# Kernel optimization log

Measured on AMD Instinct MI355X. Metric: run time of the kernel, lower is better.

Reference implementation:

```python
import jax, jax.numpy as jnp
import numpy as np

LAMBDA_LAME = 1.0
MU_LAME = 0.5
JACOBIAN_WEIGHT = 0.1
ERROR_BOUND = 0.01


def setup_inputs() -> dict:
    key = jax.random.key(0)
    df = jax.random.normal(key, (2, 3, 192, 192, 192), dtype=jnp.float32)
    return {"deformation_field": df}


def _grad(x, axis):
    # matches torch.gradient / np.gradient (edge_order=1): central diff in the
    # interior, one-sided first-order at the boundaries, unit spacing.
    return jnp.gradient(x, axis=axis)


def _robust(x, delta):
    abs_x = jnp.abs(x)
    return jnp.where(abs_x <= delta, 0.5 * x * x, delta * (abs_x - 0.5 * delta))


def reference(deformation_field):
    u = deformation_field[:, 0]  # [B, D, H, W]
    v = deformation_field[:, 1]
    w = deformation_field[:, 2]

    du_dx, du_dy, du_dz = _grad(u, 1), _grad(u, 2), _grad(u, 3)
    dv_dx, dv_dy, dv_dz = _grad(v, 1), _grad(v, 2), _grad(v, 3)
    dw_dx, dw_dy, dw_dz = _grad(w, 1), _grad(w, 2), _grad(w, 3)

    E_xx, E_yy, E_zz = du_dx, dv_dy, dw_dz
    E_xy = 0.5 * (du_dy + dv_dx)
    E_xz = 0.5 * (du_dz + dw_dx)
    E_yz = 0.5 * (dv_dz + dw_dy)
    trace_E = E_xx + E_yy + E_zz

    d = ERROR_BOUND
    tr_l = _robust(trace_E, d)
    energy = (0.5 * LAMBDA_LAME * tr_l ** 2
              + MU_LAME * (_robust(E_xx, d) ** 2 + _robust(E_yy, d) ** 2
                           + _robust(E_zz, d) ** 2
                           + 2.0 * (_robust(E_xy, d) ** 2
                                    + _robust(E_xz, d) ** 2
                                    + _robust(E_yz, d) ** 2)))

    jac = ((1 + du_dx) * ((1 + dv_dy) * (1 + dw_dz) - dv_dz * dw_dy)
           - du_dy * (dv_dx * (1 + dw_dz) - dv_dz * (1 + dw_dx))
           + du_dz * (dv_dx * dw_dy - (1 + dv_dy) * (1 + dw_dx)))
    jac_penalty = jax.nn.relu(-jac)

    total = jnp.mean(energy) + JACOBIAN_WEIGHT * jnp.mean(jac_penalty)
    return total
```

## Files before the change

kernel.cpp:

```cpp
#include <hip/hip_runtime.h>

#define DIM 192
#define PLANE (DIM * DIM)
#define VOL ((size_t)PLANE * DIM)

__device__ __forceinline__ float robustf(float x) {
    float ax = fabsf(x);
    return (ax <= 0.01f) ? (0.5f * x * x) : (0.01f * (ax - 0.005f));
}

__device__ __forceinline__ float4 ldg4(const float* __restrict__ p) {
    return *(const float4*)p;
}

__device__ __forceinline__ float4 sub_scale(float4 a, float4 b, float s) {
    return make_float4((a.x - b.x) * s, (a.y - b.y) * s,
                       (a.z - b.z) * s, (a.w - b.w) * s);
}

__device__ __forceinline__ float voxel_loss(
    float du_dx, float du_dy, float du_dz,
    float dv_dx, float dv_dy, float dv_dz,
    float dw_dx, float dw_dy, float dw_dz) {
    const float E_xy = 0.5f * (du_dy + dv_dx);
    const float E_xz = 0.5f * (du_dz + dw_dx);
    const float E_yz = 0.5f * (dv_dz + dw_dy);
    const float tr   = du_dx + dv_dy + dw_dz;

    const float rtr = robustf(tr);
    const float rxx = robustf(du_dx), ryy = robustf(dv_dy), rzz = robustf(dw_dz);
    const float rxy = robustf(E_xy),  rxz = robustf(E_xz),  ryz = robustf(E_yz);

    const float energy = 0.5f * rtr * rtr
                       + 0.5f * (rxx * rxx + ryy * ryy + rzz * rzz
                                 + 2.0f * (rxy * rxy + rxz * rxz + ryz * ryz));

    const float jac =
          (1.0f + du_dx) * ((1.0f + dv_dy) * (1.0f + dw_dz) - dv_dz * dw_dy)
        - du_dy * (dv_dx * (1.0f + dw_dz) - dv_dz * (1.0f + dw_dx))
        + du_dz * (dv_dx * dw_dy - (1.0f + dv_dy) * (1.0f + dw_dx));

    return energy + 0.1f * fmaxf(-jac, 0.0f);
}

__device__ __forceinline__ float4 zgrad(float4 c, float lf, float rt,
                                        bool leftEdge, bool rightEdge) {
    float4 g;
    g.x = leftEdge  ? (c.y - c.x) : 0.5f * (c.y - lf);
    g.y = 0.5f * (c.z - c.x);
    g.z = 0.5f * (c.w - c.y);
    g.w = rightEdge ? (c.w - c.z) : 0.5f * (rt - c.z);
    return g;
}

__global__ __launch_bounds__(256, 4)
void elastic_main(const float* __restrict__ df, double* __restrict__ acc) {
    const int tx = threadIdx.x;
    const int ty = threadIdx.y;
    const int k4 = tx * 4;
    const int j  = blockIdx.x * 4 + ty;
    const int i0 = blockIdx.y * 24;
    const int b  = blockIdx.z;

    const float* __restrict__ u = df + (size_t)(b * 3 + 0) * VOL;
    const float* __restrict__ v = df + (size_t)(b * 3 + 1) * VOL;
    const float* __restrict__ w = df + (size_t)(b * 3 + 2) * VOL;

    const int jp = (j < DIM - 1) ? j + 1 : j;
    const int jm = (j > 0) ? j - 1 : j;
    const float sy = ((jp - jm) == 2) ? 0.5f : 1.0f;

    const bool act = (tx < 48);
    const bool leftEdge  = (tx == 0);
    const bool rightEdge = (tx == 47);

    float4 um, vm, wm, uc, vc, wc;
    um = vm = wm = uc = vc = wc = make_float4(0.f, 0.f, 0.f, 0.f);

    {
        const int im1 = (i0 > 0) ? i0 - 1 : 0;
        const size_t oM = (size_t)im1 * PLANE + (size_t)j * DIM + k4;
        const size_t oC = (size_t)i0  * PLANE + (size_t)j * DIM + k4;
        if (act) {
            um = ldg4(u + oM); vm = ldg4(v + oM); wm = ldg4(w + oM);
            uc = ldg4(u + oC); vc = ldg4(v + oC); wc = ldg4(w + oC);
        }
    }

    float vsum = 0.0f;

    for (int ii = 0; ii < 24; ++ii) {
        const int i   = i0 + ii;
        const int ip1 = (i < DIM - 1) ? i + 1 : i;
        const int im1 = (i > 0) ? i - 1 : i;
        const float sx = ((ip1 - im1) == 2) ? 0.5f : 1.0f;

        const size_t oP  = (size_t)ip1 * PLANE + (size_t)j  * DIM + k4;
        const size_t oYp = (size_t)i   * PLANE + (size_t)jp * DIM + k4;
        const size_t oYm = (size_t)i   * PLANE + (size_t)jm * DIM + k4;

        float4 up, vp, wp, uyp, uym, vyp, vym, wyp, wym;
        up = vp = wp = make_float4(0.f, 0.f, 0.f, 0.f);
        if (act) {
            up  = ldg4(u + oP);  vp  = ldg4(v + oP);  wp  = ldg4(w + oP);
            uyp = ldg4(u + oYp); uym = ldg4(u + oYm);
            vyp = ldg4(v + oYp); vym = ldg4(v + oYm);
            wyp = ldg4(w + oYp); wym = ldg4(w + oYm);
        }

        const float ulf = __shfl_up(uc.w, 1);
        const float vlf = __shfl_up(vc.w, 1);
        const float wlf = __shfl_up(wc.w, 1);
        const float urt = __shfl_down(uc.x, 1);
        const float vrt = __shfl_down(vc.x, 1);
        const float wrt = __shfl_down(wc.x, 1);

        if (act) {
            const float4 du_dz = zgrad(uc, ulf, urt, leftEdge, rightEdge);
            const float4 dv_dz = zgrad(vc, vlf, vrt, leftEdge, rightEdge);
            const float4 dw_dz = zgrad(wc, wlf, wrt, leftEdge, rightEdge);

            const float4 du_dx = sub_scale(up, um, sx);
            const float4 dv_dx = sub_scale(vp, vm, sx);
            const float4 dw_dx = sub_scale(wp, wm, sx);
            const float4 du_dy = sub_scale(uyp, uym, sy);
            const float4 dv_dy = sub_scale(vyp, vym, sy);
            const float4 dw_dy = sub_scale(wyp, wym, sy);

            vsum += voxel_loss(du_dx.x, du_dy.x, du_dz.x,
                               dv_dx.x, dv_dy.x, dv_dz.x,
                               dw_dx.x, dw_dy.x, dw_dz.x);
            vsum += voxel_loss(du_dx.y, du_dy.y, du_dz.y,
                               dv_dx.y, dv_dy.y, dv_dz.y,
                               dw_dx.y, dw_dy.y, dw_dz.y);
            vsum += voxel_loss(du_dx.z, du_dy.z, du_dz.z,
                               dv_dx.z, dv_dy.z, dv_dz.z,
                               dw_dx.z, dw_dy.z, dw_dz.z);
            vsum += voxel_loss(du_dx.w, du_dy.w, du_dz.w,
                               dv_dx.w, dv_dy.w, dv_dz.w,
                               dw_dx.w, dw_dy.w, dw_dz.w);
        }

        um = uc; vm = vc; wm = wc;
        uc = up; vc = vp; wc = wp;
    }

    #pragma unroll
    for (int off = 32; off > 0; off >>= 1)
        vsum += __shfl_down(vsum, off, 64);

    __shared__ float wpart[4];
    if (tx == 0) wpart[ty] = vsum;
    __syncthreads();
    if (tx == 0 && ty == 0) {
        double s = (double)wpart[0] + (double)wpart[1]
                 + (double)wpart[2] + (double)wpart[3];
        unsafeAtomicAdd(acc, s);
    }
}

__global__ void elastic_finalize(const double* __restrict__ acc, float* __restrict__ out) {
    out[0] = (float)(acc[0] * (1.0 / 14155776.0));
}

extern "C" void kernel_launch(void* const* d_in, const int* in_sizes, int n_in,
                              void* d_out, int out_size, void* d_ws, size_t ws_size,
                              hipStream_t stream) {
    const float* df = (const float*)d_in[0];
    double* acc = (double*)d_ws;
    float* out = (float*)d_out;

    hipMemsetAsync(d_ws, 0, sizeof(double), stream);

    dim3 grid(48, 8, 2);
    dim3 block(64, 4);
    elastic_main<<<grid, block, 0, stream>>>(df, acc);
    elastic_finalize<<<1, 1, 0, stream>>>(acc, out);
}
```

Before: 254.5 us.

## Replace atomic accumulation with per-block partials and double the x-slab depth

Each block now writes its partial sum to its own slot in the workspace, and a 256-thread finalize kernel reduces those partials. This removes the memset launch and the global double atomics. Each block also marches through 48 x-planes instead of 24, which halves the grid to 384 blocks and cuts redundant halo loads, but gives less parallelism across the GPU's compute units.

New measurement: 283.7 us. +11.5%, slower.

```diff
diff --git a/kernel.cpp b/kernel.cpp
--- a/kernel.cpp
+++ b/kernel.cpp
@@ -3,6 +3,7 @@
 #define DIM 192
 #define PLANE (DIM * DIM)
 #define VOL ((size_t)PLANE * DIM)
+#define NBLK 384
 
 __device__ __forceinline__ float robustf(float x) {
     float ax = fabsf(x);
@@ -54,12 +55,12 @@
 }
 
 __global__ __launch_bounds__(256, 4)
-void elastic_main(const float* __restrict__ df, double* __restrict__ acc) {
+void elastic_main(const float* __restrict__ df, double* __restrict__ partial) {
     const int tx = threadIdx.x;
     const int ty = threadIdx.y;
     const int k4 = tx * 4;
     const int j  = blockIdx.x * 4 + ty;
-    const int i0 = blockIdx.y * 24;
+    const int i0 = blockIdx.y * 48;
     const int b  = blockIdx.z;
 
     const float* __restrict__ u = df + (size_t)(b * 3 + 0) * VOL;
@@ -89,7 +90,7 @@
 
     float vsum = 0.0f;
 
-    for (int ii = 0; ii < 24; ++ii) {
+    for (int ii = 0; ii < 48; ++ii) {
         const int i   = i0 + ii;
         const int ip1 = (i < DIM - 1) ? i + 1 : i;
         const int im1 = (i > 0) ? i - 1 : i;
@@ -153,27 +154,39 @@
     if (tx == 0) wpart[ty] = vsum;
     __syncthreads();
     if (tx == 0 && ty == 0) {
-        double s = (double)wpart[0] + (double)wpart[1]
-                 + (double)wpart[2] + (double)wpart[3];
-        unsafeAtomicAdd(acc, s);
+        const int blk = blockIdx.x + 48 * (blockIdx.y + 4 * blockIdx.z);
+        partial[blk] = (double)wpart[0] + (double)wpart[1]
+                     + (double)wpart[2] + (double)wpart[3];
     }
 }
 
-__global__ void elastic_finalize(const double* __restrict__ acc, float* __restrict__ out) {
-    out[0] = (float)(acc[0] * (1.0 / 14155776.0));
+__global__ __launch_bounds__(256)
+void elastic_finalize(const double* __restrict__ partial, float* __restrict__ out) {
+    const int t = threadIdx.x;
+    double s = partial[t] + ((t < NBLK - 256) ? partial[t + 256] : 0.0);
+
+    #pragma unroll
+    for (int off = 32; off > 0; off >>= 1)
+        s += __shfl_down(s, off, 64);
+
+    __shared__ double wpart[4];
+    if ((t & 63) == 0) wpart[t >> 6] = s;
+    __syncthreads();
+    if (t == 0) {
+        double tot = wpart[0] + wpart[1] + wpart[2] + wpart[3];
+        out[0] = (float)(tot * (1.0 / 14155776.0));
+    }
 }
 
 extern "C" void kernel_launch(void* const* d_in, const int* in_sizes, int n_in,
                               void* d_out, int out_size, void* d_ws, size_t ws_size,
                               hipStream_t stream) {
     const float* df = (const float*)d_in[0];
-    double* acc = (double*)d_ws;
+    double* partial = (double*)d_ws;
     float* out = (float*)d_out;
 
-    hipMemsetAsync(d_ws, 0, sizeof(double), stream);
-
-    dim3 grid(48, 8, 2);
+    dim3 grid(48, 4, 2);
     dim3 block(64, 4);
-    elastic_main<<<grid, block, 0, stream>>>(df, acc);
-    elastic_finalize<<<1, 1, 0, stream>>>(acc, out);
+    elastic_main<<<grid, block, 0, stream>>>(df, partial);
+    elastic_finalize<<<1, 256, 0, stream>>>(partial, out);
 }
```
